# Performance work log

Measured on AMD Instinct MI355X. Metric: run time of the kernel, lower is better.

The kernel has to match this reference:

```python
import jax, jax.numpy as jnp
import numpy as np

B, N, D, E = 256, 192, 512, 1024
H = E // 2          # MLP hidden = 512
K = 58              # round(0.3 * 192), hardcoded in the torch forward
EPS_L2 = 1e-8
EPS_BN = 1e-5


def setup_inputs() -> dict:
    key = jax.random.key(0)
    ks = jax.random.split(key, 8)
    s = 0.02
    return {
        "all_patch_embeddings": jax.random.normal(ks[0], (B, N, D), dtype=jnp.float32),
        "attention_map": jax.random.uniform(ks[1], (B, N + 1, N + 1), dtype=jnp.float32),
        # fc: Linear(D, E)
        "W_fc": jax.random.normal(ks[2], (E, D), dtype=jnp.float32) * s,
        "b_fc": jnp.zeros((E,), dtype=jnp.float32),
        # mlp layer 0: Linear(D, H) + BatchNorm1d(H) + ReLU
        "W1": jax.random.normal(ks[3], (H, D), dtype=jnp.float32) * s,
        "b1": jnp.zeros((H,), dtype=jnp.float32),
        "gamma1": jnp.ones((H,), dtype=jnp.float32),
        "beta1": jnp.zeros((H,), dtype=jnp.float32),
        # mlp layer 1: Linear(H, E) (no BN/ReLU applied on last layer)
        "W2": jax.random.normal(ks[4], (E, H), dtype=jnp.float32) * s,
        "b2": jnp.zeros((E,), dtype=jnp.float32),
    }


def reference(all_patch_embeddings, attention_map, W_fc, b_fc, W1, b1, gamma1, beta1, W2, b2):
    # CLS-row attention over the 192 patch tokens: [B, N]
    cls_attn = attention_map[:, 0, 1:]
    # torch.sort(descending)[...,:K] == top-k indices (batched, replaces python loop)
    _, idx = jax.lax.top_k(cls_attn, K)                      # [B, K] int32
    # batched gather replacing the per-sample index_select loop
    sel = jnp.take_along_axis(all_patch_embeddings, idx[:, :, None], axis=1)  # [B, K, D]
    # l2norm over last dim
    norm = jnp.sqrt(jnp.sum(sel * sel, axis=-1, keepdims=True)) + EPS_L2
    base = sel / norm
    # .half() cast in the original (round-trip to fp16 precision)
    base = base.astype(jnp.float16).astype(jnp.float32)
    # fc branch
    feat_fc = jnp.einsum('bkd,ed->bke', base, W_fc) + b_fc    # [B, K, E]
    # mlp branch (num_layers=2): Linear -> BN(train-mode batch stats) -> ReLU -> Linear
    h = jnp.einsum('bkd,hd->bkh', base, W1) + b1              # [B, K, H]
    hf = h.reshape(B * K, H)
    mu = jnp.mean(hf, axis=0)
    var = jnp.var(hf, axis=0)
    hf = (hf - mu) * jax.lax.rsqrt(var + EPS_BN) * gamma1 + beta1
    h = jax.nn.relu(hf).reshape(B, K, H)
    feat_mlp = jnp.einsum('bkh,eh->bke', h, W2) + b2          # [B, K, E]
    feats = feat_mlp + feat_fc
    # maxk_pool1d_var with k=1 and lengths == K reduces to max over token dim
    return jnp.max(feats, axis=1).astype(jnp.float32)         # [B, E]
```

## Files before the change

kernel.cpp:

```cpp
#include <hip/hip_runtime.h>
#include <hip/hip_fp16.h>

#define B_ 256
#define N_ 192
#define D_ 512
#define E_ 1024
#define H_ 512
#define K_ 58
#define M_ (B_*K_)
#define M2_ (B_*64)

typedef _Float16 f16;
typedef unsigned int u32;
typedef _Float16 half8 __attribute__((ext_vector_type(8)));
typedef float floatx4 __attribute__((ext_vector_type(4)));

__device__ inline half8 cvt8(float4 f0, float4 f1) {
  half8 r;
  r[0]=(f16)f0.x; r[1]=(f16)f0.y; r[2]=(f16)f0.z; r[3]=(f16)f0.w;
  r[4]=(f16)f1.x; r[5]=(f16)f1.y; r[6]=(f16)f1.z; r[7]=(f16)f1.w;
  return r;
}

__device__ inline void gl_lds16(const f16* g, f16* l) {
  __builtin_amdgcn_global_load_lds((const __attribute__((address_space(1))) u32*)g,
                                   (__attribute__((address_space(3))) u32*)l, 16, 0, 0);
}

__device__ inline void stage128(const f16* gbase, int gstride, f16* sT, int w, int lane) {
  int lrow  = lane >> 2;
  int chunk = (lane & 3) ^ ((lane >> 3) & 3);
  gl_lds16(gbase + (size_t)(w*16      + lrow)*gstride + chunk*8, &sT[(w*16)*32]);
  gl_lds16(gbase + (size_t)(64 + w*16 + lrow)*gstride + chunk*8, &sT[(64 + w*16)*32]);
}
__device__ inline void stage256(const f16* gbase, int gstride, f16* sT, int w, int lane) {
  int lrow  = lane >> 2;
  int chunk = (lane & 3) ^ ((lane >> 3) & 3);
  #pragma unroll
  for (int q = 0; q < 4; ++q)
    gl_lds16(gbase + (size_t)(q*64 + w*16 + lrow)*gstride + chunk*8, &sT[(q*64 + w*16)*32]);
}

__global__ void setup_kernel(const float* __restrict__ Wfc, const float* __restrict__ W2,
                             const float* __restrict__ W1, const float* __restrict__ attn,
                             const float* __restrict__ emb,
                             f16* __restrict__ Wcat, f16* __restrict__ W1_16,
                             f16* __restrict__ A16, float* __restrict__ csum) {
  __shared__ float sv[N_];
  __shared__ int sidx[K_];
  __shared__ int cnt;
  int blk = blockIdx.x, t = threadIdx.x;
  if (blk < 512) {
    int idx = (blk*256 + t)*8;
    int e = idx >> 10, c = idx & 1023;
    const float* src = (c < 512) ? (Wfc + (size_t)e*512 + c)
                                 : (W2  + (size_t)e*512 + (c-512));
    half8 o = cvt8(((const float4*)src)[0], ((const float4*)src)[1]);
    *(uint4*)(Wcat + idx) = *(uint4*)&o;
  } else if (blk < 640) {
    int idx = ((blk-512)*256 + t)*8;
    const float* src = W1 + idx;
    half8 o = cvt8(((const float4*)src)[0], ((const float4*)src)[1]);
    *(uint4*)(W1_16 + idx) = *(uint4*)&o;
  } else if (blk < 896) {
    int b = blk - 640;
    if (t == 0) cnt = 0;
    if (t < N_) sv[t] = attn[(size_t)b*193*193 + 1 + t];
    __syncthreads();
    if (t < N_) {
      float v = sv[t]; int rank = 0;
      for (int j = 0; j < N_; ++j) {
        float vj = sv[j];
        rank += (vj > v) || (vj == v && j < t);
      }
      if (rank < K_) sidx[atomicAdd(&cnt, 1)] = t;
    }
    __syncthreads();
    int w = t >> 6, lane = t & 63;
    for (int slot = w; slot < 64; slot += 4) {
      f16* dst = A16 + ((size_t)b*64 + slot)*1024 + lane*8;
      if (slot < K_) {
        const float* src = emb + ((size_t)b*N_ + sidx[slot])*D_ + lane*8;
        float4 v0 = ((const float4*)src)[0];
        float4 v1 = ((const float4*)src)[1];
        float s = v0.x*v0.x + v0.y*v0.y + v0.z*v0.z + v0.w*v0.w
                + v1.x*v1.x + v1.y*v1.y + v1.z*v1.z + v1.w*v1.w;
        #pragma unroll
        for (int off = 32; off > 0; off >>= 1) s += __shfl_xor(s, off);
        float inv = 1.0f / (sqrtf(s) + 1e-8f);
        half8 o;
        o[0]=(f16)(v0.x*inv); o[1]=(f16)(v0.y*inv); o[2]=(f16)(v0.z*inv); o[3]=(f16)(v0.w*inv);
        o[4]=(f16)(v1.x*inv); o[5]=(f16)(v1.y*inv); o[6]=(f16)(v1.z*inv); o[7]=(f16)(v1.w*inv);
        *(uint4*)dst = *(uint4*)&o;
      } else {
        uint4 z; z.x=0u; z.y=0u; z.z=0u; z.w=0u;
        *(uint4*)dst = z;
      }
    }
  } else {
    float4 z; z.x=0.f; z.y=0.f; z.z=0.f; z.w=0.f;
    ((float4*)csum)[t] = z;
  }
}

__launch_bounds__(256, 2)
__global__ void gemm1_kernel(const f16* __restrict__ A16, const f16* __restrict__ W1_16,
                             const float* __restrict__ b1, f16* __restrict__ Aout,
                             float* __restrict__ csum, float* __restrict__ css) {
  __shared__ f16 sA[2][128*32];
  __shared__ f16 sB[2][256*32];
  __shared__ float sSum[4][128], sSS[4][128];
  int t = threadIdx.x;
  int g = blockIdx.x;
  int xcd = g & 7, rest = g >> 3;
  int n0 = (rest & 1) * 256;
  int m  = xcd + 8*(rest >> 1);
  int m0 = m * 128;
  int lane = t & 63, w = t >> 6, lm = lane & 15, quad = lane >> 4;
  int rw = w & 1, cw = w >> 1;
  floatx4 acc[4][8] = {};
  const f16* Ab = A16 + (size_t)m0*1024;
  const f16* Bb = W1_16 + (size_t)n0*512;
  int sw = (quad ^ ((lm >> 1) & 3)) * 8;
  stage128(Ab, 1024, sA[0], w, lane);
  stage256(Bb, 512,  sB[0], w, lane);
  __syncthreads();
  for (int it = 0; it < 16; ++it) {
    int cur = it & 1, nxt = cur ^ 1;
    if (it < 15) {
      stage128(Ab + (it+1)*32, 1024, sA[nxt], w, lane);
      stage256(Bb + (it+1)*32, 512,  sB[nxt], w, lane);
    }
    half8 a[4], bf[8];
    #pragma unroll
    for (int i = 0; i < 4; ++i) a[i]  = *(const half8*)&sA[cur][(rw*64  + i*16 + lm)*32 + sw];
    #pragma unroll
    for (int j = 0; j < 8; ++j) bf[j] = *(const half8*)&sB[cur][(cw*128 + j*16 + lm)*32 + sw];
    #pragma unroll
    for (int i = 0; i < 4; ++i)
      #pragma unroll
      for (int j = 0; j < 8; ++j)
        acc[i][j] = __builtin_amdgcn_mfma_f32_16x16x32_f16(a[i], bf[j], acc[i][j], 0, 0, 0);
    __syncthreads();
  }
  #pragma unroll
  for (int j = 0; j < 8; ++j) {
    int col = n0 + cw*128 + j*16 + lm;
    float bias = b1[col];
    float s = 0.f, ss = 0.f;
    #pragma unroll
    for (int i = 0; i < 4; ++i) {
      int rib = i*16 + quad*4;
      int row = m0 + rw*64 + rib;
      #pragma unroll
      for (int r = 0; r < 4; ++r) {
        float x = acc[i][j][r] + bias;
        Aout[(size_t)(row + r)*1024 + 512 + col] = (f16)x;
        if (rib + r < K_) { s += x; ss += x*x; }
      }
    }
    s  += __shfl_xor(s, 16);  s  += __shfl_xor(s, 32);
    ss += __shfl_xor(ss, 16); ss += __shfl_xor(ss, 32);
    if (lane < 16) { sSum[w][j*16 + lm] = s; sSS[w][j*16 + lm] = ss; }
  }
  __syncthreads();
  {
    int c = t;
    int w0 = 2*(c >> 7), ci = c & 127;
    atomicAdd(&csum[n0 + c], sSum[w0][ci] + sSum[w0+1][ci]);
    atomicAdd(&css[n0 + c],  sSS[w0][ci]  + sSS[w0+1][ci]);
  }
}

__global__ void bnrelu_kernel(f16* __restrict__ A16, const float* __restrict__ csum,
                              const float* __restrict__ css, const float* __restrict__ gamma,
                              const float* __restrict__ beta) {
  __shared__ float sSc[H_], sSh[H_];
  int t = threadIdx.x;
  for (int j = t; j < H_; j += 256) {
    float mu  = csum[j] * (1.0f/M_);
    float var = css[j] * (1.0f/M_) - mu*mu;
    float sc  = gamma[j] * rsqrtf(var + 1e-5f);
    sSc[j] = sc;
    sSh[j] = beta[j] - mu*sc;
  }
  __syncthreads();
  int r0 = blockIdx.x * 16;
  #pragma unroll
  for (int i = 0; i < 4; ++i) {
    int seg = t + 256*i;
    int row = r0 + (seg >> 6);
    int c0  = (seg & 63) * 8;
    f16* p = A16 + (size_t)row*1024 + 512 + c0;
    if ((row & 63) >= K_) {
      uint4 z; z.x=0u; z.y=0u; z.z=0u; z.w=0u;
      *(uint4*)p = z;
    } else {
      half8 hv = *(const half8*)p;
      half8 o;
      #pragma unroll
      for (int k = 0; k < 8; ++k)
        o[k] = (f16)fmaxf((float)hv[k]*sSc[c0+k] + sSh[c0+k], 0.0f);
      *(uint4*)p = *(uint4*)&o;
    }
  }
}

__launch_bounds__(256, 2)
__global__ void fused_kernel(const f16* __restrict__ A16, const f16* __restrict__ Wcat,
                             const float* __restrict__ bfc, const float* __restrict__ b2,
                             float* __restrict__ out) {
  __shared__ f16 sA[2][128*32];
  __shared__ f16 sB[2][256*32];
  __shared__ float sMax[4][128];
  int t = threadIdx.x;
  int g = blockIdx.x;
  int xcd = g & 7, rest = g >> 3;
  int e0 = (rest & 3) * 256;
  int bm = xcd + 8*(rest >> 2);
  int lane = t & 63, w = t >> 6, lm = lane & 15, quad = lane >> 4;
  int rw = w & 1, cw = w >> 1;
  floatx4 acc[4][8] = {};
  const f16* Ab = A16 + (size_t)bm*128*1024;
  const f16* Bb = Wcat + (size_t)e0*1024;
  int sw = (quad ^ ((lm >> 1) & 3)) * 8;
  stage128(Ab, 1024, sA[0], w, lane);
  stage256(Bb, 1024, sB[0], w, lane);
  __syncthreads();
  for (int it = 0; it < 32; ++it) {
    int cur = it & 1, nxt = cur ^ 1;
    if (it < 31) {
      stage128(Ab + (it+1)*32, 1024, sA[nxt], w, lane);
      stage256(Bb + (it+1)*32, 1024, sB[nxt], w, lane);
    }
    half8 a[4], bf[8];
    #pragma unroll
    for (int i = 0; i < 4; ++i) a[i]  = *(const half8*)&sA[cur][(rw*64  + i*16 + lm)*32 + sw];
    #pragma unroll
    for (int j = 0; j < 8; ++j) bf[j] = *(const half8*)&sB[cur][(cw*128 + j*16 + lm)*32 + sw];
    #pragma unroll
    for (int i = 0; i < 4; ++i)
      #pragma unroll
      for (int j = 0; j < 8; ++j)
        acc[i][j] = __builtin_amdgcn_mfma_f32_16x16x32_f16(a[i], bf[j], acc[i][j], 0, 0, 0);
    __syncthreads();
  }
  #pragma unroll
  for (int j = 0; j < 8; ++j) {
    float mx = -3.0e38f;
    #pragma unroll
    for (int i = 0; i < 4; ++i) {
      int rib = i*16 + quad*4;
      #pragma unroll
      for (int r = 0; r < 4; ++r)
        if (rib + r < K_) mx = fmaxf(mx, acc[i][j][r]);
    }
    mx = fmaxf(mx, __shfl_xor(mx, 16));
    mx = fmaxf(mx, __shfl_xor(mx, 32));
    if (lane < 16) sMax[w][j*16 + lm] = mx;
  }
  __syncthreads();
  #pragma unroll
  for (int bb = 0; bb < 2; ++bb) {
    int c = t;
    float mx = sMax[bb + 2*(c >> 7)][c & 127];
    int e = e0 + c;
    out[((size_t)bm*2 + bb)*E_ + e] = mx + bfc[e] + b2[e];
  }
}

extern "C" void kernel_launch(void* const* d_in, const int* in_sizes, int n_in,
                              void* d_out, int out_size, void* d_ws, size_t ws_size,
                              hipStream_t stream) {
  const float* emb   = (const float*)d_in[0];
  const float* attn  = (const float*)d_in[1];
  const float* Wfc   = (const float*)d_in[2];
  const float* bfc   = (const float*)d_in[3];
  const float* W1    = (const float*)d_in[4];
  const float* b1    = (const float*)d_in[5];
  const float* gamma = (const float*)d_in[6];
  const float* beta  = (const float*)d_in[7];
  const float* W2    = (const float*)d_in[8];
  const float* b2    = (const float*)d_in[9];
  float* out = (float*)d_out;

  char* ws = (char*)d_ws;
  f16*   A16   = (f16*)(ws);
  f16*   Wcat  = (f16*)(ws + 33554432);
  f16*   W1_16 = (f16*)(ws + 35651584);
  float* csum  = (float*)(ws + 36175872);
  float* css   = (float*)(ws + 36177920);

  setup_kernel<<<897, 256, 0, stream>>>(Wfc, W2, W1, attn, emb, Wcat, W1_16, A16, csum);
  gemm1_kernel<<<256, 256, 0, stream>>>(A16, W1_16, b1, A16, csum, css);
  bnrelu_kernel<<<M2_/16, 256, 0, stream>>>(A16, csum, css, gamma, beta);
  fused_kernel<<<512, 256, 0, stream>>>(A16, Wcat, bfc, b2, out);
}
```

Measured before the change: 248.6 us.

## Fuse BatchNorm+ReLU into the final GEMM's A-tile staging

Removes the separate bnrelu kernel. The fused GEMM now computes the BN scale and shift per block from the column sums and applies BN, ReLU and pad-row zeroing while loading the hidden half of the A operand. Those tiles go through registers into LDS instead of the async LDS path. This saves one launch and a full read-modify-write of the hidden activations, but the in-loop global loads and ALU work may stall the MFMA pipeline, and every one of the 512 blocks recomputes the BN parameters.

```diff
diff --git a/kernel.cpp b/kernel.cpp
--- a/kernel.cpp
+++ b/kernel.cpp
@@ -172,46 +172,15 @@
   }
 }
 
-__global__ void bnrelu_kernel(f16* __restrict__ A16, const float* __restrict__ csum,
-                              const float* __restrict__ css, const float* __restrict__ gamma,
-                              const float* __restrict__ beta) {
-  __shared__ float sSc[H_], sSh[H_];
-  int t = threadIdx.x;
-  for (int j = t; j < H_; j += 256) {
-    float mu  = csum[j] * (1.0f/M_);
-    float var = css[j] * (1.0f/M_) - mu*mu;
-    float sc  = gamma[j] * rsqrtf(var + 1e-5f);
-    sSc[j] = sc;
-    sSh[j] = beta[j] - mu*sc;
-  }
-  __syncthreads();
-  int r0 = blockIdx.x * 16;
-  #pragma unroll
-  for (int i = 0; i < 4; ++i) {
-    int seg = t + 256*i;
-    int row = r0 + (seg >> 6);
-    int c0  = (seg & 63) * 8;
-    f16* p = A16 + (size_t)row*1024 + 512 + c0;
-    if ((row & 63) >= K_) {
-      uint4 z; z.x=0u; z.y=0u; z.z=0u; z.w=0u;
-      *(uint4*)p = z;
-    } else {
-      half8 hv = *(const half8*)p;
-      half8 o;
-      #pragma unroll
-      for (int k = 0; k < 8; ++k)
-        o[k] = (f16)fmaxf((float)hv[k]*sSc[c0+k] + sSh[c0+k], 0.0f);
-      *(uint4*)p = *(uint4*)&o;
-    }
-  }
-}
-
 __launch_bounds__(256, 2)
 __global__ void fused_kernel(const f16* __restrict__ A16, const f16* __restrict__ Wcat,
+                             const float* __restrict__ csum, const float* __restrict__ css,
+                             const float* __restrict__ gamma, const float* __restrict__ beta,
                              const float* __restrict__ bfc, const float* __restrict__ b2,
                              float* __restrict__ out) {
   __shared__ f16 sA[2][128*32];
   __shared__ f16 sB[2][256*32];
+  __shared__ float sSc[H_], sSh[H_];
   __shared__ float sMax[4][128];
   int t = threadIdx.x;
   int g = blockIdx.x;
@@ -220,18 +189,41 @@
   int bm = xcd + 8*(rest >> 2);
   int lane = t & 63, w = t >> 6, lm = lane & 15, quad = lane >> 4;
   int rw = w & 1, cw = w >> 1;
+  #pragma unroll
+  for (int jj = 0; jj < 2; ++jj) {
+    int j = t + jj*256;
+    float mu  = csum[j] * (1.0f/M_);
+    float var = css[j] * (1.0f/M_) - mu*mu;
+    float sc  = gamma[j] * rsqrtf(var + 1e-5f);
+    sSc[j] = sc;
+    sSh[j] = beta[j] - mu*sc;
+  }
   floatx4 acc[4][8] = {};
   const f16* Ab = A16 + (size_t)bm*128*1024;
   const f16* Bb = Wcat + (size_t)e0*1024;
   int sw = (quad ^ ((lm >> 1) & 3)) * 8;
+  int rr = t >> 2;
+  int rslot  = (t & 3) * 8;
+  int rchunk = (t & 3) ^ ((t >> 3) & 3);
+  bool pad = (rr >= K_);
   stage128(Ab, 1024, sA[0], w, lane);
   stage256(Bb, 1024, sB[0], w, lane);
   __syncthreads();
   for (int it = 0; it < 32; ++it) {
     int cur = it & 1, nxt = cur ^ 1;
+    int kn = (it + 1) * 32;
+    uint4 h0, h1;
+    bool regp = false;
     if (it < 31) {
-      stage128(Ab + (it+1)*32, 1024, sA[nxt], w, lane);
-      stage256(Bb + (it+1)*32, 1024, sB[nxt], w, lane);
+      stage256(Bb + kn, 1024, sB[nxt], w, lane);
+      if (kn < 512) {
+        stage128(Ab + kn, 1024, sA[nxt], w, lane);
+      } else {
+        regp = true;
+        const f16* hp = Ab + (size_t)rr*1024 + kn + rchunk*8;
+        h0 = *(const uint4*)hp;
+        h1 = *(const uint4*)(hp + (size_t)64*1024);
+      }
     }
     half8 a[4], bf[8];
     #pragma unroll
@@ -243,6 +235,35 @@
       #pragma unroll
       for (int j = 0; j < 8; ++j)
         acc[i][j] = __builtin_amdgcn_mfma_f32_16x16x32_f16(a[i], bf[j], acc[i][j], 0, 0, 0);
+    if (regp) {
+      int cb = kn - 512 + rchunk*8;
+      float4 sc0 = *(float4*)&sSc[cb], sc1 = *(float4*)&sSc[cb+4];
+      float4 sh0 = *(float4*)&sSh[cb], sh1 = *(float4*)&sSh[cb+4];
+      half8 v0 = *(half8*)&h0, v1 = *(half8*)&h1;
+      half8 o0, o1;
+      o0[0]=(f16)fmaxf((float)v0[0]*sc0.x+sh0.x, 0.f);
+      o0[1]=(f16)fmaxf((float)v0[1]*sc0.y+sh0.y, 0.f);
+      o0[2]=(f16)fmaxf((float)v0[2]*sc0.z+sh0.z, 0.f);
+      o0[3]=(f16)fmaxf((float)v0[3]*sc0.w+sh0.w, 0.f);
+      o0[4]=(f16)fmaxf((float)v0[4]*sc1.x+sh1.x, 0.f);
+      o0[5]=(f16)fmaxf((float)v0[5]*sc1.y+sh1.y, 0.f);
+      o0[6]=(f16)fmaxf((float)v0[6]*sc1.z+sh1.z, 0.f);
+      o0[7]=(f16)fmaxf((float)v0[7]*sc1.w+sh1.w, 0.f);
+      o1[0]=(f16)fmaxf((float)v1[0]*sc0.x+sh0.x, 0.f);
+      o1[1]=(f16)fmaxf((float)v1[1]*sc0.y+sh0.y, 0.f);
+      o1[2]=(f16)fmaxf((float)v1[2]*sc0.z+sh0.z, 0.f);
+      o1[3]=(f16)fmaxf((float)v1[3]*sc0.w+sh0.w, 0.f);
+      o1[4]=(f16)fmaxf((float)v1[4]*sc1.x+sh1.x, 0.f);
+      o1[5]=(f16)fmaxf((float)v1[5]*sc1.y+sh1.y, 0.f);
+      o1[6]=(f16)fmaxf((float)v1[6]*sc1.z+sh1.z, 0.f);
+      o1[7]=(f16)fmaxf((float)v1[7]*sc1.w+sh1.w, 0.f);
+      if (pad) {
+        uint4 z; z.x=0u; z.y=0u; z.z=0u; z.w=0u;
+        *(uint4*)&o0 = z; *(uint4*)&o1 = z;
+      }
+      *(uint4*)&sA[nxt][rr*32 + rslot]        = *(uint4*)&o0;
+      *(uint4*)&sA[nxt][(64 + rr)*32 + rslot] = *(uint4*)&o1;
+    }
     __syncthreads();
   }
   #pragma unroll
@@ -293,6 +314,5 @@
 
   setup_kernel<<<897, 256, 0, stream>>>(Wfc, W2, W1, attn, emb, Wcat, W1_16, A16, csum);
   gemm1_kernel<<<256, 256, 0, stream>>>(A16, W1_16, b1, A16, csum, css);
-  bnrelu_kernel<<<M2_/16, 256, 0, stream>>>(A16, csum, css, gamma, beta);
-  fused_kernel<<<512, 256, 0, stream>>>(A16, Wcat, bfc, b2, out);
-}
+  fused_kernel<<<512, 256, 0, stream>>>(A16, Wcat, csum, css, gamma, beta, bfc, b2, out);
+}
```

New measurement: 243.4 us. 2.1% less time.
